# Optimization experiments

Measured on AMD Instinct MI355X. Metric: run time of the kernel, lower is better.

## Reference

```python
import jax, jax.numpy as jnp
import numpy as np

B, S, D, H, FF = 4, 2048, 1024, 16, 4096
DT, TARGET, ITERS = 0.1, 0.0, 5


def _ln(x, w, b):
    mu = jnp.mean(x, axis=-1, keepdims=True)
    var = jnp.mean((x - mu) ** 2, axis=-1, keepdims=True)
    return (x - mu) * jax.lax.rsqrt(var + 1e-5) * w + b


def setup_inputs() -> dict:
    key = jax.random.key(0)
    ks = iter(jax.random.split(key, 16))
    w = lambda shape: jax.random.normal(next(ks), shape, dtype=jnp.float32) * 0.02
    return {
        "x": jax.random.normal(next(ks), (B, S, D), dtype=jnp.float32),
        "ln_attn_w": jnp.ones((D,), jnp.float32), "ln_attn_b": jnp.zeros((D,), jnp.float32),
        "attn_in_w": w((3 * D, D)), "attn_in_b": jnp.zeros((3 * D,), jnp.float32),
        "attn_out_w": w((D, D)), "attn_out_b": jnp.zeros((D,), jnp.float32),
        "ln1_w": jnp.ones((D,), jnp.float32), "ln1_b": jnp.zeros((D,), jnp.float32),
        "ln2_w": jnp.ones((D,), jnp.float32), "ln2_b": jnp.zeros((D,), jnp.float32),
        "inl_u_w": w((D, D)), "inl_u_b": jnp.zeros((D,), jnp.float32),
        "inl_a_w": w((D, D)), "inl_a_b": jnp.zeros((D,), jnp.float32),
        "inl_b_w": w((D, D)), "inl_b_b": jnp.zeros((D,), jnp.float32),
        "inl_g_w": w((D, D)), "inl_g_b": jnp.zeros((D,), jnp.float32),
        "ff1_w": w((FF, D)), "ff1_b": jnp.zeros((FF,), jnp.float32),
        "ff2_w": w((D, FF)), "ff2_b": jnp.zeros((D,), jnp.float32),
    }


def reference(x, ln_attn_w, ln_attn_b, attn_in_w, attn_in_b, attn_out_w, attn_out_b,
              ln1_w, ln1_b, ln2_w, ln2_b,
              inl_u_w, inl_u_b, inl_a_w, inl_a_b, inl_b_w, inl_b_b, inl_g_w, inl_g_b,
              ff1_w, ff1_b, ff2_w, ff2_b):
    dh = D // H
    scale = 1.0 / np.sqrt(dh).astype(np.float32)
    # --- causal multi-head attention (dropout = identity, eval mode) ---
    xn = _ln(x, ln_attn_w, ln_attn_b)
    qkv = xn @ attn_in_w.T + attn_in_b            # [B,S,3D]
    q, k, v = jnp.split(qkv, 3, axis=-1)
    hsplit = lambda t: t.reshape(B, S, H, dh).transpose(0, 2, 1, 3)  # [B,H,S,dh]
    q, k, v = hsplit(q), hsplit(k), hsplit(v)
    scores = jnp.einsum('bhqd,bhkd->bhqk', q, k) * scale
    causal = jnp.triu(jnp.ones((S, S), dtype=bool), 1)
    scores = jnp.where(causal, jnp.finfo(scores.dtype).min, scores)
    probs = jax.nn.softmax(scores, axis=-1)
    attn_out = jnp.einsum('bhqk,bhkd->bhqd', probs, v).transpose(0, 2, 1, 3).reshape(B, S, D)
    attn_out = attn_out @ attn_out_w.T + attn_out_b
    x = x + attn_out
    context = attn_out
    # --- INL integrator dynamics (controllers depend only on context) ---
    xs = _ln(x, ln1_w, ln1_b)
    vs = jnp.zeros_like(xs)
    u = context @ inl_u_w.T + inl_u_b
    alpha = jax.nn.sigmoid(context @ inl_a_w.T + inl_a_b)
    beta = jax.nn.softplus(context @ inl_b_w.T + inl_b_b)
    g = jax.nn.sigmoid(context @ inl_g_w.T + inl_g_b)
    for _ in range(ITERS):
        vs = vs + DT * (alpha * (TARGET - xs) - beta * vs + u)
        xs = xs + DT * g * vs
    x = x + xs
    # --- feed-forward (exact GELU as torch default) ---
    h = _ln(x, ln2_w, ln2_b)
    x = x + (jax.nn.gelu(h @ ff1_w.T + ff1_b, approximate=False) @ ff2_w.T + ff2_b)
    return x
```

## Files before the change

kernel.cpp:

```cpp
#include <hip/hip_runtime.h>
#include <cstdint>
#include <cmath>

typedef __attribute__((ext_vector_type(4))) float floatx4;
typedef __attribute__((ext_vector_type(8))) __bf16 bf16x8;
typedef __attribute__((ext_vector_type(4))) unsigned short ushort4v;

#define DEVI static __device__ __forceinline__

DEVI unsigned short f2b(float f) {
    unsigned x = __float_as_uint(f);
    return (unsigned short)((x + 0x7fffu + ((x >> 16) & 1u)) >> 16);
}
DEVI float b2f(unsigned short u) { return __uint_as_float(((unsigned)u) << 16); }

DEVI void load16(void* lds, const void* g) {
    __builtin_amdgcn_global_load_lds(
        (__attribute__((address_space(1))) void*)(const_cast<void*>(g)),
        (__attribute__((address_space(3))) void*)lds, 16, 0, 0);
}

__global__ __launch_bounds__(256) void cvt_kernel(const float* __restrict__ src,
                                                  unsigned short* __restrict__ dst, int n4) {
    int i = blockIdx.x * 256 + threadIdx.x;
    if (i >= n4) return;
    floatx4 v = ((const floatx4*)src)[i];
    ushort4v o;
    o[0] = f2b(v[0]); o[1] = f2b(v[1]); o[2] = f2b(v[2]); o[3] = f2b(v[3]);
    ((ushort4v*)dst)[i] = o;
}

__global__ __launch_bounds__(256) void catbias_kernel(const float* __restrict__ a,
                                                      const float* __restrict__ b,
                                                      const float* __restrict__ c,
                                                      const float* __restrict__ d,
                                                      float* __restrict__ o) {
    int i = blockIdx.x * 256 + threadIdx.x;
    int p = i >> 10, j = i & 1023;
    float v = (p == 0) ? a[j] : (p == 1) ? b[j] : (p == 2) ? c[j] : d[j];
    o[i] = v;
}

__global__ __launch_bounds__(256) void ln_kernel(const float* __restrict__ in,
                                                 const float* __restrict__ w,
                                                 const float* __restrict__ b,
                                                 unsigned short* __restrict__ obf,
                                                 float* __restrict__ of) {
    const int row = blockIdx.x, tid = threadIdx.x;
    const floatx4* pr = (const floatx4*)(in + (size_t)row * 1024);
    floatx4 v = pr[tid];
    float s  = v[0] + v[1] + v[2] + v[3];
    float ss = v[0]*v[0] + v[1]*v[1] + v[2]*v[2] + v[3]*v[3];
    #pragma unroll
    for (int o = 32; o >= 1; o >>= 1) { s += __shfl_xor(s, o); ss += __shfl_xor(ss, o); }
    __shared__ float red[8];
    int wv = tid >> 6, lane = tid & 63;
    if (lane == 0) { red[wv] = s; red[4 + wv] = ss; }
    __syncthreads();
    s  = red[0] + red[1] + red[2] + red[3];
    ss = red[4] + red[5] + red[6] + red[7];
    float mu  = s * (1.0f / 1024.0f);
    float var = ss * (1.0f / 1024.0f) - mu * mu;
    float rstd = rsqrtf(var + 1e-5f);
    floatx4 wv4 = ((const floatx4*)w)[tid];
    floatx4 bv4 = ((const floatx4*)b)[tid];
    floatx4 o;
    #pragma unroll
    for (int c = 0; c < 4; c++) o[c] = (v[c] - mu) * rstd * wv4[c] + bv4[c];
    if (obf) {
        ushort4v t;
        t[0] = f2b(o[0]); t[1] = f2b(o[1]); t[2] = f2b(o[2]); t[3] = f2b(o[3]);
        ((ushort4v*)(obf + (size_t)row * 1024))[tid] = t;
    }
    if (of) ((floatx4*)(of + (size_t)row * 1024))[tid] = o;
}

__global__ __launch_bounds__(256) void integrator_kernel(const float* __restrict__ xs0,
                                                         const unsigned short* __restrict__ uabg,
                                                         float* __restrict__ xio) {
    size_t i = (size_t)blockIdx.x * 256 + threadIdx.x;
    size_t tok = i >> 8;
    int grp = (int)(i & 255) * 4;
    const unsigned short* ubase = uabg + tok * 4096 + grp;
    ushort4v uu = *(const ushort4v*)(ubase);
    ushort4v aa = *(const ushort4v*)(ubase + 1024);
    ushort4v bb = *(const ushort4v*)(ubase + 2048);
    ushort4v gg = *(const ushort4v*)(ubase + 3072);
    floatx4 xsv = ((const floatx4*)xs0)[i];
    floatx4 x1  = ((const floatx4*)xio)[i];
    floatx4 res;
    #pragma unroll
    for (int c = 0; c < 4; c++) {
        float u = b2f(uu[c]), a = b2f(aa[c]), bt = b2f(bb[c]), g = b2f(gg[c]);
        float xs = xsv[c], vs = 0.f;
        #pragma unroll
        for (int t = 0; t < 5; t++) {
            vs += 0.1f * (-a * xs - bt * vs + u);
            xs += 0.1f * g * vs;
        }
        res[c] = x1[c] + xs;
    }
    ((floatx4*)xio)[i] = res;
}

template <int EPI>
__global__ __launch_bounds__(256) void gemm_bt(const unsigned short* __restrict__ A,
                                               const unsigned short* __restrict__ W,
                                               const float* __restrict__ bias, int K,
                                               unsigned short* __restrict__ ob0,
                                               unsigned short* __restrict__ ob1,
                                               unsigned short* __restrict__ ob2,
                                               float* __restrict__ of0,
                                               const float* __restrict__ xres) {
    __shared__ unsigned short sA[2][128 * 32];
    __shared__ unsigned short sB[2][128 * 32];
    const int tid = threadIdx.x;
    const int wave = tid >> 6, lane = tid & 63;
    const int ln = lane & 15, quad = lane >> 4;
    const size_t m0 = (size_t)blockIdx.y * 128;
    const int n0 = blockIdx.x * 128;
    const int wm = (wave >> 1) * 64, wn = (wave & 1) * 64;

    const floatx4 z4 = {0.f, 0.f, 0.f, 0.f};
    floatx4 acc[4][4];
    #pragma unroll
    for (int mt = 0; mt < 4; mt++)
        #pragma unroll
        for (int nt = 0; nt < 4; nt++) acc[mt][nt] = z4;

    const int r16 = lane >> 2;
    const int gsw = ((lane & 3) ^ (r16 & 3)) * 8;
    const int arow = wave * 16 + r16;
    const unsigned short* gA = A + (m0 + (size_t)arow) * K + gsw;
    const unsigned short* gB = W + ((size_t)(n0 + arow)) * K + gsw;
    const size_t rs64 = (size_t)64 * K;
    const int so = wave * 512;

    load16(&sA[0][so], gA);
    load16(&sA[0][so + 2048], gA + rs64);
    load16(&sB[0][so], gB);
    load16(&sB[0][so + 2048], gB + rs64);

    const int T = K >> 5;
    const int swr = (quad ^ (ln & 3)) * 8;

    #pragma unroll 1
    for (int t = 0; t < T; t++) {
        const int cur = t & 1;
        if (t + 1 < T) {
            const int k = (t + 1) * 32;
            load16(&sA[cur ^ 1][so], gA + k);
            load16(&sA[cur ^ 1][so + 2048], gA + rs64 + k);
            load16(&sB[cur ^ 1][so], gB + k);
            load16(&sB[cur ^ 1][so + 2048], gB + rs64 + k);
            asm volatile("s_waitcnt vmcnt(4)" ::: "memory");
        } else {
            asm volatile("s_waitcnt vmcnt(0)" ::: "memory");
        }
        asm volatile("s_barrier" ::: "memory");

        bf16x8 af[4], bfr[4];
        #pragma unroll
        for (int mt = 0; mt < 4; mt++)
            af[mt] = *(const bf16x8*)&sA[cur][(wm + mt * 16 + ln) * 32 + swr];
        #pragma unroll
        for (int nt = 0; nt < 4; nt++)
            bfr[nt] = *(const bf16x8*)&sB[cur][(wn + nt * 16 + ln) * 32 + swr];
        #pragma unroll
        for (int mt = 0; mt < 4; mt++)
            #pragma unroll
            for (int nt = 0; nt < 4; nt++)
                acc[mt][nt] = __builtin_amdgcn_mfma_f32_16x16x32_bf16(af[mt], bfr[nt], acc[mt][nt], 0, 0, 0);

        asm volatile("s_waitcnt lgkmcnt(0)" ::: "memory");
        asm volatile("s_barrier" ::: "memory");
    }

    const size_t rowb = m0 + wm + quad * 4;
    const int colb = n0 + wn + ln;
    #pragma unroll
    for (int mt = 0; mt < 4; mt++) {
        #pragma unroll
        for (int nt = 0; nt < 4; nt++) {
            const int n = colb + nt * 16;
            const float bs = bias[n];
            #pragma unroll
            for (int r = 0; r < 4; r++) {
                const size_t row = rowb + mt * 16 + r;
                float c = acc[mt][nt][r] + bs;
                if constexpr (EPI == 0) {
                    int sect = n >> 10, d1 = n & 1023, h = d1 >> 6, d = d1 & 63;
                    int bb = (int)(row >> 11), s = (int)(row & 2047);
                    size_t bh = (size_t)(bb * 16 + h);
                    if (sect == 0)      ob0[(bh * 2048 + s) * 64 + d] = f2b(c);
                    else if (sect == 1) ob1[(bh * 2048 + s) * 64 + d] = f2b(c);
                    else                ob2[(bh * 64 + d) * 2048 + s] = f2b(c);
                } else if constexpr (EPI == 1) {
                    size_t idx = row * 1024 + n;
                    ob0[idx] = f2b(c);
                    of0[idx] = xres[idx] + c;
                } else if constexpr (EPI == 2) {
                    int p = n >> 10;
                    float v;
                    if (p == 0)       v = c;
                    else if (p == 2)  v = fmaxf(c, 0.f) + log1pf(__expf(-fabsf(c)));
                    else              v = 1.f / (1.f + __expf(-c));
                    ob0[row * 4096 + n] = f2b(v);
                } else if constexpr (EPI == 3) {
                    float v = 0.5f * c * (1.f + erff(c * 0.70710678118654752f));
                    ob0[row * 4096 + n] = f2b(v);
                } else {
                    size_t idx = row * 1024 + n;
                    of0[idx] += c;
                }
            }
        }
    }
}

#define PSTR 72
__global__ __launch_bounds__(256, 3) void attn_kernel(const unsigned short* __restrict__ Qb,
                                                      const unsigned short* __restrict__ Kb,
                                                      const unsigned short* __restrict__ Vtb,
                                                      unsigned short* __restrict__ Ob) {
    __shared__ unsigned short sK[2][64 * 64];
    __shared__ unsigned short sVt[2][64 * 64];
    __shared__ unsigned short sQP[128 * PSTR];
    const int pr = blockIdx.x;
    const int bh = blockIdx.y;
    const int tid = threadIdx.x, wave = tid >> 6, lane = tid & 63;
    const int ln = lane & 15, quad = lane >> 4;
    const unsigned short* Q  = Qb  + (size_t)bh * 2048 * 64;
    const unsigned short* Kp = Kb  + (size_t)bh * 2048 * 64;
    const unsigned short* Vt = Vtb + (size_t)bh * 64 * 2048;

    const int rl  = lane >> 3;
    const int gsw = (((lane & 7) ^ rl)) * 8;
    const int sseg = wave * 2;
    const unsigned short* kbase = Kp + (size_t)(sseg * 8 + rl) * 64 + gsw;
    const unsigned short* vbase = Vt + (size_t)(sseg * 8 + rl) * 2048 + gsw;
    unsigned short* sP = &sQP[wave * 32 * PSTR];
    const int bb = bh >> 4, h = bh & 15;
    const floatx4 z4 = {0.f, 0.f, 0.f, 0.f};

    #pragma unroll 1
    for (int phase = 0; phase < 2; phase++) {
        const int qt = phase ? pr : (15 - pr);
        const int q0 = qt * 128;
        const int T = 2 * qt + 2;

        #pragma unroll
        for (int i = 0; i < 4; i++) {
            int s = wave * 4 + i;
            load16(&sQP[s * 512], Q + (size_t)(q0 + s * 8 + rl) * 64 + gsw);
        }
        load16(&sK[0][sseg * 512], kbase);
        load16(&sK[0][(sseg + 1) * 512], kbase + (size_t)8 * 64);
        load16(&sVt[0][sseg * 512], vbase);
        load16(&sVt[0][(sseg + 1) * 512], vbase + (size_t)8 * 2048);
        asm volatile("s_waitcnt vmcnt(0)" ::: "memory");
        asm volatile("s_barrier" ::: "memory");

        bf16x8 aq[2][2];
        #pragma unroll
        for (int mt = 0; mt < 2; mt++)
            #pragma unroll
            for (int ks = 0; ks < 2; ks++)
                aq[mt][ks] = *(const bf16x8*)&sQP[(wave * 32 + mt * 16 + ln) * 64 +
                                                  (((ks * 4 + quad) ^ (ln & 7)) * 8)];
        asm volatile("s_waitcnt lgkmcnt(0)" ::: "memory");
        asm volatile("s_barrier" ::: "memory");

        floatx4 Oacc[2][4];
        float m_run[2][4], l_run[2][4];
        #pragma unroll
        for (int mt = 0; mt < 2; mt++)
            #pragma unroll
            for (int j = 0; j < 4; j++) { Oacc[mt][j] = z4; m_run[mt][j] = -1e30f; l_run[mt][j] = 0.f; }

        const int wave_first = q0 + wave * 32;
        const int wave_last  = wave_first + 31;

        #pragma unroll 1
        for (int t = 0; t < T; t++) {
            const int kk0 = t * 64;
            const int cur = t & 1;
            if (t + 1 < T) {
                const unsigned short* kg = kbase + (size_t)(kk0 + 64) * 64;
                const unsigned short* vg = vbase + (size_t)(kk0 + 64);
                load16(&sK[cur ^ 1][sseg * 512], kg);
                load16(&sK[cur ^ 1][(sseg + 1) * 512], kg + (size_t)8 * 64);
                load16(&sVt[cur ^ 1][sseg * 512], vg);
                load16(&sVt[cur ^ 1][(sseg + 1) * 512], vg + (size_t)8 * 2048);
                asm volatile("s_waitcnt vmcnt(4)" ::: "memory");
            } else {
                asm volatile("s_waitcnt vmcnt(0)" ::: "memory");
            }
            asm volatile("s_barrier" ::: "memory");

            if (kk0 <= wave_last) {
                floatx4 Sc[2][4];
                #pragma unroll
                for (int mt = 0; mt < 2; mt++)
                    #pragma unroll
                    for (int nt = 0; nt < 4; nt++) Sc[mt][nt] = z4;
                #pragma unroll
                for (int ks = 0; ks < 2; ks++) {
                    #pragma unroll
                    for (int nt = 0; nt < 4; nt++) {
                        bf16x8 bk = *(const bf16x8*)&sK[cur][(nt * 16 + ln) * 64 +
                                                             (((ks * 4 + quad) ^ (ln & 7)) * 8)];
                        #pragma unroll
                        for (int mt = 0; mt < 2; mt++)
                            Sc[mt][nt] = __builtin_amdgcn_mfma_f32_16x16x32_bf16(aq[mt][ks], bk, Sc[mt][nt], 0, 0, 0);
                    }
                }
                const bool diag = (kk0 + 63 > wave_first);
                #pragma unroll
                for (int mt = 0; mt < 2; mt++)
                    #pragma unroll
                    for (int nt = 0; nt < 4; nt++)
                        #pragma unroll
                        for (int r = 0; r < 4; r++) {
                            float v = Sc[mt][nt][r] * 0.125f;
                            if (diag) {
                                int rowg = wave_first + mt * 16 + quad * 4 + r;
                                int colg = kk0 + nt * 16 + ln;
                                if (colg > rowg) v = -1e30f;
                            }
                            Sc[mt][nt][r] = v;
                        }
                float alpha[2][4];
                #pragma unroll
                for (int mt = 0; mt < 2; mt++)
                    #pragma unroll
                    for (int r = 0; r < 4; r++) {
                        float mx = fmaxf(fmaxf(Sc[mt][0][r], Sc[mt][1][r]), fmaxf(Sc[mt][2][r], Sc[mt][3][r]));
                        #pragma unroll
                        for (int off = 1; off < 16; off <<= 1) mx = fmaxf(mx, __shfl_xor(mx, off));
                        float mnew = fmaxf(m_run[mt][r], mx);
                        alpha[mt][r] = __expf(m_run[mt][r] - mnew);
                        m_run[mt][r] = mnew;
                    }
                #pragma unroll
                for (int mt = 0; mt < 2; mt++)
                    #pragma unroll
                    for (int r = 0; r < 4; r++) {
                        float rs = 0.f;
                        #pragma unroll
                        for (int nt = 0; nt < 4; nt++) {
                            float p = __expf(Sc[mt][nt][r] - m_run[mt][r]);
                            Sc[mt][nt][r] = p;
                            rs += p;
                        }
                        #pragma unroll
                        for (int off = 1; off < 16; off <<= 1) rs += __shfl_xor(rs, off);
                        l_run[mt][r] = l_run[mt][r] * alpha[mt][r] + rs;
                    }
                #pragma unroll
                for (int mt = 0; mt < 2; mt++)
                    #pragma unroll
                    for (int nt = 0; nt < 4; nt++)
                        #pragma unroll
                        for (int r = 0; r < 4; r++) Oacc[mt][nt][r] *= alpha[mt][r];
                #pragma unroll
                for (int mt = 0; mt < 2; mt++)
                    #pragma unroll
                    for (int nt = 0; nt < 4; nt++)
                        #pragma unroll
                        for (int r = 0; r < 4; r++)
                            sP[(mt * 16 + quad * 4 + r) * PSTR + nt * 16 + ln] = f2b(Sc[mt][nt][r]);
                #pragma unroll
                for (int kp = 0; kp < 2; kp++) {
                    bf16x8 ap[2];
                    #pragma unroll
                    for (int mt = 0; mt < 2; mt++)
                        ap[mt] = *(const bf16x8*)&sP[(mt * 16 + ln) * PSTR + kp * 32 + quad * 8];
                    #pragma unroll
                    for (int nt = 0; nt < 4; nt++) {
                        bf16x8 bv = *(const bf16x8*)&sVt[cur][(nt * 16 + ln) * 64 +
                                                              (((kp * 4 + quad) ^ (ln & 7)) * 8)];
                        #pragma unroll
                        for (int mt = 0; mt < 2; mt++)
                            Oacc[mt][nt] = __builtin_amdgcn_mfma_f32_16x16x32_bf16(ap[mt], bv, Oacc[mt][nt], 0, 0, 0);
                    }
                }
            }
            asm volatile("s_barrier" ::: "memory");
        }

        #pragma unroll
        for (int mt = 0; mt < 2; mt++)
            #pragma unroll
            for (int nt = 0; nt < 4; nt++)
                #pragma unroll
                for (int r = 0; r < 4; r++) {
                    float o = Oacc[mt][nt][r] / l_run[mt][r];
                    int srow = q0 + wave * 32 + mt * 16 + quad * 4 + r;
                    size_t tok = (size_t)bb * 2048 + srow;
                    Ob[tok * 1024 + h * 64 + nt * 16 + ln] = f2b(o);
                }
    }
}

extern "C" void kernel_launch(void* const* d_in, const int* in_sizes, int n_in,
                              void* d_out, int out_size, void* d_ws, size_t ws_size,
                              hipStream_t stream) {
    const float* x          = (const float*)d_in[0];
    const float* ln_attn_w  = (const float*)d_in[1];
    const float* ln_attn_b  = (const float*)d_in[2];
    const float* attn_in_w  = (const float*)d_in[3];
    const float* attn_in_b  = (const float*)d_in[4];
    const float* attn_out_w = (const float*)d_in[5];
    const float* attn_out_b = (const float*)d_in[6];
    const float* ln1_w      = (const float*)d_in[7];
    const float* ln1_b      = (const float*)d_in[8];
    const float* ln2_w      = (const float*)d_in[9];
    const float* ln2_b      = (const float*)d_in[10];
    const float* inl_u_w    = (const float*)d_in[11];
    const float* inl_u_b    = (const float*)d_in[12];
    const float* inl_a_w    = (const float*)d_in[13];
    const float* inl_a_b    = (const float*)d_in[14];
    const float* inl_b_w    = (const float*)d_in[15];
    const float* inl_b_b    = (const float*)d_in[16];
    const float* inl_g_w    = (const float*)d_in[17];
    const float* inl_g_b    = (const float*)d_in[18];
    const float* ff1_w      = (const float*)d_in[19];
    const float* ff1_b      = (const float*)d_in[20];
    const float* ff2_w      = (const float*)d_in[21];
    const float* ff2_b      = (const float*)d_in[22];
    float* out = (float*)d_out;

    char* ws = (char*)d_ws;
    unsigned short* Wqkv  = (unsigned short*)(ws);
    unsigned short* Wout  = (unsigned short*)(ws + 6291456);
    unsigned short* Winl  = (unsigned short*)(ws + 8388608);
    unsigned short* Wff1  = (unsigned short*)(ws + 16777216);
    unsigned short* Wff2  = (unsigned short*)(ws + 25165824);
    unsigned short* xnb   = (unsigned short*)(ws + 33554432);
    unsigned short* qb    = (unsigned short*)(ws + 50331648);
    unsigned short* kb    = (unsigned short*)(ws + 67108864);
    unsigned short* vtb   = (unsigned short*)(ws + 83886080);
    unsigned short* attnb = (unsigned short*)(ws + 100663296);
    unsigned short* ctxb  = (unsigned short*)(ws + 117440512);
    float*          xs    = (float*)(ws + 134217728);
    float*          bias4 = (float*)(ws + 167772160);
    unsigned short* uabg  = (unsigned short*)(ws + 50331648);
    unsigned short* ff1b  = (unsigned short*)(ws + 50331648);

    cvt_kernel<<<3072, 256, 0, stream>>>(attn_in_w, Wqkv, 786432);
    cvt_kernel<<<1024, 256, 0, stream>>>(attn_out_w, Wout, 262144);
    cvt_kernel<<<1024, 256, 0, stream>>>(inl_u_w, Winl + 0, 262144);
    cvt_kernel<<<1024, 256, 0, stream>>>(inl_a_w, Winl + 1048576, 262144);
    cvt_kernel<<<1024, 256, 0, stream>>>(inl_b_w, Winl + 2097152, 262144);
    cvt_kernel<<<1024, 256, 0, stream>>>(inl_g_w, Winl + 3145728, 262144);
    cvt_kernel<<<4096, 256, 0, stream>>>(ff1_w, Wff1, 1048576);
    cvt_kernel<<<4096, 256, 0, stream>>>(ff2_w, Wff2, 1048576);
    catbias_kernel<<<16, 256, 0, stream>>>(inl_u_b, inl_a_b, inl_b_b, inl_g_b, bias4);

    ln_kernel<<<8192, 256, 0, stream>>>(x, ln_attn_w, ln_attn_b, xnb, nullptr);
    gemm_bt<0><<<dim3(24, 64), 256, 0, stream>>>(xnb, Wqkv, attn_in_b, 1024, qb, kb, vtb, nullptr, nullptr);
    attn_kernel<<<dim3(8, 64), 256, 0, stream>>>(qb, kb, vtb, attnb);
    gemm_bt<1><<<dim3(8, 64), 256, 0, stream>>>(attnb, Wout, attn_out_b, 1024, ctxb, nullptr, nullptr, out, x);
    ln_kernel<<<8192, 256, 0, stream>>>(out, ln1_w, ln1_b, nullptr, xs);
    gemm_bt<2><<<dim3(32, 64), 256, 0, stream>>>(ctxb, Winl, bias4, 1024, uabg, nullptr, nullptr, nullptr, nullptr);
    integrator_kernel<<<8192, 256, 0, stream>>>(xs, uabg, out);
    ln_kernel<<<8192, 256, 0, stream>>>(out, ln2_w, ln2_b, xnb, nullptr);
    gemm_bt<3><<<dim3(32, 64), 256, 0, stream>>>(xnb, Wff1, ff1_b, 1024, ff1b, nullptr, nullptr, nullptr, nullptr);
    gemm_bt<4><<<dim3(8, 64), 256, 0, stream>>>(ff1b, Wff2, ff2_b, 4096, nullptr, nullptr, nullptr, out, nullptr);
}
```

Measured before the change: 890.3 us.

## Triple-buffer GEMM LDS tiles and register-prefetch next k-fragment

The bf16 GEMM main loop moves from double-buffered LDS with two barriers per k-step to a three-stage LDS ring with one barrier per step. Fragments for the next k-step are read into a second register set while the MFMAs run on the current one. The goal is to hide global-load and LDS-read latency behind the matrix ops and remove a barrier per iteration. In exchange it uses 50% more LDS and more registers, which may lower occupancy, and the loop assumes T is even.

```diff
diff --git a/kernel.cpp b/kernel.cpp
--- a/kernel.cpp
+++ b/kernel.cpp
@@ -112,8 +112,8 @@
                                                unsigned short* __restrict__ ob2,
                                                float* __restrict__ of0,
                                                const float* __restrict__ xres) {
-    __shared__ unsigned short sA[2][128 * 32];
-    __shared__ unsigned short sB[2][128 * 32];
+    __shared__ unsigned short sA[3][128 * 32];
+    __shared__ unsigned short sB[3][128 * 32];
     const int tid = threadIdx.x;
     const int wave = tid >> 6, lane = tid & 63;
     const int ln = lane & 15, quad = lane >> 4;
@@ -135,45 +135,64 @@
     const unsigned short* gB = W + ((size_t)(n0 + arow)) * K + gsw;
     const size_t rs64 = (size_t)64 * K;
     const int so = wave * 512;
+    const int swr = (quad ^ (ln & 3)) * 8;
+
+    const int T = K >> 5;
 
     load16(&sA[0][so], gA);
     load16(&sA[0][so + 2048], gA + rs64);
     load16(&sB[0][so], gB);
     load16(&sB[0][so + 2048], gB + rs64);
-
-    const int T = K >> 5;
-    const int swr = (quad ^ (ln & 3)) * 8;
+    load16(&sA[1][so], gA + 32);
+    load16(&sA[1][so + 2048], gA + rs64 + 32);
+    load16(&sB[1][so], gB + 32);
+    load16(&sB[1][so + 2048], gB + rs64 + 32);
+    asm volatile("s_waitcnt vmcnt(4)" ::: "memory");
+    asm volatile("s_barrier" ::: "memory");
+
+    bf16x8 fa0[4], fb0[4], fa1[4], fb1[4];
+    #pragma unroll
+    for (int mt = 0; mt < 4; mt++)
+        fa0[mt] = *(const bf16x8*)&sA[0][(wm + mt * 16 + ln) * 32 + swr];
+    #pragma unroll
+    for (int nt = 0; nt < 4; nt++)
+        fb0[nt] = *(const bf16x8*)&sB[0][(wn + nt * 16 + ln) * 32 + swr];
+
+    auto step = [&](int t, bf16x8* afc, bf16x8* bfc, bf16x8* afn, bf16x8* bfn) {
+        if (t + 2 < T) {
+            const int k = (t + 2) * 32;
+            const int nb = (t + 2) % 3;
+            load16(&sA[nb][so], gA + k);
+            load16(&sA[nb][so + 2048], gA + rs64 + k);
+            load16(&sB[nb][so], gB + k);
+            load16(&sB[nb][so + 2048], gB + rs64 + k);
+            asm volatile("s_waitcnt vmcnt(4) lgkmcnt(0)" ::: "memory");
+        } else if (t + 1 < T) {
+            asm volatile("s_waitcnt vmcnt(0) lgkmcnt(0)" ::: "memory");
+        } else {
+            asm volatile("s_waitcnt lgkmcnt(0)" ::: "memory");
+        }
+        asm volatile("s_barrier" ::: "memory");
+        if (t + 1 < T) {
+            const int nb = (t + 1) % 3;
+            #pragma unroll
+            for (int mt = 0; mt < 4; mt++)
+                afn[mt] = *(const bf16x8*)&sA[nb][(wm + mt * 16 + ln) * 32 + swr];
+            #pragma unroll
+            for (int nt = 0; nt < 4; nt++)
+                bfn[nt] = *(const bf16x8*)&sB[nb][(wn + nt * 16 + ln) * 32 + swr];
+        }
+        #pragma unroll
+        for (int mt = 0; mt < 4; mt++)
+            #pragma unroll
+            for (int nt = 0; nt < 4; nt++)
+                acc[mt][nt] = __builtin_amdgcn_mfma_f32_16x16x32_bf16(afc[mt], bfc[nt], acc[mt][nt], 0, 0, 0);
+    };
 
     #pragma unroll 1
-    for (int t = 0; t < T; t++) {
-        const int cur = t & 1;
-        if (t + 1 < T) {
-            const int k = (t + 1) * 32;
-            load16(&sA[cur ^ 1][so], gA + k);
-            load16(&sA[cur ^ 1][so + 2048], gA + rs64 + k);
-            load16(&sB[cur ^ 1][so], gB + k);
-            load16(&sB[cur ^ 1][so + 2048], gB + rs64 + k);
-            asm volatile("s_waitcnt vmcnt(4)" ::: "memory");
-        } else {
-            asm volatile("s_waitcnt vmcnt(0)" ::: "memory");
-        }
-        asm volatile("s_barrier" ::: "memory");
-
-        bf16x8 af[4], bfr[4];
-        #pragma unroll
-        for (int mt = 0; mt < 4; mt++)
-            af[mt] = *(const bf16x8*)&sA[cur][(wm + mt * 16 + ln) * 32 + swr];
-        #pragma unroll
-        for (int nt = 0; nt < 4; nt++)
-            bfr[nt] = *(const bf16x8*)&sB[cur][(wn + nt * 16 + ln) * 32 + swr];
-        #pragma unroll
-        for (int mt = 0; mt < 4; mt++)
-            #pragma unroll
-            for (int nt = 0; nt < 4; nt++)
-                acc[mt][nt] = __builtin_amdgcn_mfma_f32_16x16x32_bf16(af[mt], bfr[nt], acc[mt][nt], 0, 0, 0);
-
-        asm volatile("s_waitcnt lgkmcnt(0)" ::: "memory");
-        asm volatile("s_barrier" ::: "memory");
+    for (int t = 0; t < T; t += 2) {
+        step(t, fa0, fb0, fa1, fb1);
+        step(t + 1, fa1, fb1, fa0, fb0);
     }
 
     const size_t rowb = m0 + wm + quad * 4;
```

Result: faster. 871.4 us (-2.1%).
